# Kernel tuning notes

Hardware: AMD Instinct MI355X
Metric: run time of the kernel (lower is better)

The kernel has to match this reference:

```python
import jax, jax.numpy as jnp
import numpy as np

RADIUS = 4
SIGMA1 = 5.0
SIGMA2 = 1.0


def _gauss_1d(radius, sigma):
    x = jnp.arange(-radius, radius + 1, dtype=jnp.float32)
    return jnp.exp(-(x ** 2) / (2.0 * sigma ** 2))  # peak-1 gaussian (norm.pdf(d)/norm.pdf(0))


def _blur3d(x, g, radius):
    # Separable 3D gaussian conv; product of 1D kernels == exp(-(dx^2+dy^2+dz^2)/(2*sigma^2)),
    # mathematically identical to the dense (2r+1)^3 conv3d in the torch module.
    dn = ('NCDHW', 'OIDHW', 'NCDHW')
    for ax in range(3):
        shape = [1, 1, 1, 1, 1]
        shape[2 + ax] = g.shape[0]
        k = g.reshape(shape)
        pad = [(0, 0), (0, 0), (0, 0)]
        pad[ax] = (radius, radius)
        x = jax.lax.conv_general_dilated(x, k, (1, 1, 1), pad, dimension_numbers=dn)
    return x


def setup_inputs() -> dict:
    key = jax.random.key(0)
    k1, k2 = jax.random.split(key)
    labels = jax.random.uniform(k1, (2, 4, 128, 128, 128), dtype=jnp.float32)
    inputs = jax.random.normal(k2, (2, 1, 128, 128, 128), dtype=jnp.float32)
    return {"labels": labels, "inputs": inputs}


def reference(labels, inputs):
    num_classes = labels.shape[1]
    g = _gauss_1d(RADIUS, SIGMA1)
    loss = jnp.float32(0.0)
    for k in range(num_classes):
        class_probs = labels[:, k:k + 1]  # [B,1,D,H,W]
        class_mean = (jnp.mean(inputs * class_probs, axis=(2, 3, 4), keepdims=True)
                      / (jnp.mean(class_probs, axis=(2, 3, 4), keepdims=True) + 1e-5))  # [B,C,1,1,1]
        diff = jnp.sum((inputs - class_mean) ** 2, axis=1, keepdims=True)  # [B,1,D,H,W]
        weights = jnp.exp(-(diff ** 2) / (SIGMA2 ** 2))
        numerator = jnp.sum(class_probs * _blur3d(class_probs * weights, g, RADIUS))
        denominator = jnp.sum(class_probs * _blur3d(weights, g, RADIUS))
        # L1Loss(x, 0) on a scalar == |x|
        loss = loss + jnp.abs(numerator / (denominator + 1e-6))
    return num_classes - loss
```

## Files before the change

### kernel.cpp

```cpp
#include <hip/hip_runtime.h>
#include <math.h>

#define DIM   128
#define SLICE (DIM*DIM)
#define VOL   (DIM*DIM*DIM)
#define NK    4
#define NVOL  8
#define SSTR  33

__constant__ float c_g[9] = {
    0.72614904f, 0.83527021f, 0.92311635f, 0.98019867f, 1.0f,
    0.98019867f, 0.92311635f, 0.83527021f, 0.72614904f
};


__global__ __launch_bounds__(256) void k_sums(
    const float* __restrict__ labels, const float* __restrict__ inputs,
    float* __restrict__ red)
{
    const int b     = blockIdx.x >> 9;
    const int chunk = blockIdx.x & 511;
    const int t     = threadIdx.x;
    const size_t off4 = (size_t)chunk*1024 + t;
    const float4* __restrict__ I4 = (const float4*)inputs + (size_t)b*(VOL/4) + off4;
    const float4* __restrict__ L4 = (const float4*)labels;
    float sp[4] = {0,0,0,0}, sip[4] = {0,0,0,0};
    #pragma unroll
    for (int j = 0; j < 4; ++j) {
        const float4 iv = I4[j*256];
        #pragma unroll
        for (int k = 0; k < 4; ++k) {
            const float4 p = L4[(size_t)(b*NK + k)*(VOL/4) + off4 + j*256];
            sp[k]  += p.x + p.y + p.z + p.w;
            sip[k] += p.x*iv.x + p.y*iv.y + p.z*iv.z + p.w*iv.w;
        }
    }
    #pragma unroll
    for (int k = 0; k < 4; ++k) {
        #pragma unroll
        for (int o = 32; o; o >>= 1) {
            sp[k]  += __shfl_down(sp[k],  o);
            sip[k] += __shfl_down(sip[k], o);
        }
    }
    __shared__ float sB[8][4];
    const int wid = t >> 6;
    if ((t & 63) == 0) {
        #pragma unroll
        for (int k = 0; k < 4; ++k) { sB[k][wid] = sp[k]; sB[4+k][wid] = sip[k]; }
    }
    __syncthreads();
    if (t < 8) {
        const float v = sB[t][0] + sB[t][1] + sB[t][2] + sB[t][3];
        atomicAdd(&red[(t < 4 ? 0 : 8) + b*NK + (t & 3)], v);
    }
}

__global__ __launch_bounds__(256) void k_fused(
    const float* __restrict__ labels, const float* __restrict__ inputs,
    const float* __restrict__ red, float* __restrict__ nd)
{
    __shared__ float4 sW[2][16*SSTR + 8];
    __shared__ float sN[4], sD[4];

    const int dq    = blockIdx.x & 3;
    const int strip = (blockIdx.x >> 2) & 15;
    const int vol   = blockIdx.x >> 6;
    const int b = vol >> 2, kcls = vol & 3;
    const int d0 = dq * 32;
    const int t  = threadIdx.x;
    const float g1 = c_g[5], g2 = c_g[6], g3 = c_g[7], g4 = c_g[8];
    const float4 z4 = make_float4(0.f, 0.f, 0.f, 0.f);

    const float* __restrict__ src = labels + (size_t)vol*VOL;
    const float mean = red[8+vol] / (red[vol] + 20.97152f);

    const int r0 = t >> 5, c0 = t & 31;
    const int r1 = r0 + 8;
    const int ho = t >> 5, wq = t & 31;

    const int hA = strip*8 - 4 + r0;
    const int hB = strip*8 - 4 + r1;
    const bool vA = (unsigned)hA < 128u;
    const bool vB = (unsigned)hB < 128u;
    const float4* __restrict__ rowA = (const float4*)(src + (size_t)(vA ? hA : 0)*DIM);
    const float4* __restrict__ rowB = (const float4*)(src + (size_t)(vB ? hB : 0)*DIM);

    const size_t ob4 = (size_t)(strip*8 + ho)*(DIM/4) + wq;
    const float4* __restrict__ P4 = (const float4*)src + ob4;
    const float4* __restrict__ I4 = (const float4*)(inputs + (size_t)b*VOL) + ob4;

    float4 ring[9];
    #pragma unroll
    for (int i = 0; i < 9; ++i) ring[i] = z4;
    float numAcc = 0.f, denAcc = 0.f;

    auto ldA = [&](int s, float4& pv, float4& cv, float4& nx) {
        pv = cv = nx = z4;
        if (vA && (unsigned)s < 128u) {
            const float4* rp = rowA + (size_t)s*(SLICE/4);
            cv = rp[c0];
            if (c0 > 0)  pv = rp[c0-1];
            if (c0 < 31) nx = rp[c0+1];
        }
    };
    auto ldB = [&](int s, float4& pv, float4& cv, float4& nx) {
        pv = cv = nx = z4;
        if (vB && (unsigned)s < 128u) {
            const float4* rp = rowB + (size_t)s*(SLICE/4);
            cv = rp[c0];
            if (c0 > 0)  pv = rp[c0-1];
            if (c0 < 31) nx = rp[c0+1];
        }
    };

    float4 Apv, Acv, Anx, Bpv, Bcv, Bnx;
    ldA(d0-4, Apv, Acv, Anx);
    ldB(d0-4, Bpv, Bcv, Bnx);

    #pragma unroll 2
    for (int s = d0-4; s < d0+36; ++s) {
        const float4 apv=Apv, acv=Acv, anx=Anx, bpv=Bpv, bcv=Bcv, bnx=Bnx;
        ldA(s+1, Apv, Acv, Anx);
        ldB(s+1, Bpv, Bcv, Bnx);
        float4 pc = z4, ic = z4;
        const bool outStep = (s >= d0+4);
        if (outStep) {
            pc = P4[(size_t)(s-4)*(SLICE/4)];
            ic = I4[(size_t)(s-4)*(SLICE/4)];
        }
        const int buf = s & 1;
        {
            float4 o;
            o.x = acv.x + g1*(apv.w+acv.y) + g2*(apv.z+acv.z) + g3*(apv.y+acv.w) + g4*(apv.x+anx.x);
            o.y = acv.y + g1*(acv.x+acv.z) + g2*(apv.w+acv.w) + g3*(apv.z+anx.x) + g4*(apv.y+anx.y);
            o.z = acv.z + g1*(acv.y+acv.w) + g2*(acv.x+anx.x) + g3*(apv.w+anx.y) + g4*(apv.z+anx.z);
            o.w = acv.w + g1*(acv.z+anx.x) + g2*(acv.y+anx.y) + g3*(acv.x+anx.z) + g4*(apv.w+anx.w);
            sW[buf][r0*SSTR + c0] = o;
        }
        {
            float4 o;
            o.x = bcv.x + g1*(bpv.w+bcv.y) + g2*(bpv.z+bcv.z) + g3*(bpv.y+bcv.w) + g4*(bpv.x+bnx.x);
            o.y = bcv.y + g1*(bcv.x+bcv.z) + g2*(bpv.w+bcv.w) + g3*(bpv.z+bnx.x) + g4*(bpv.y+bnx.y);
            o.z = bcv.z + g1*(bcv.y+bcv.w) + g2*(bcv.x+bnx.x) + g3*(bpv.w+bnx.y) + g4*(bpv.z+bnx.z);
            o.w = bcv.w + g1*(bcv.z+bnx.x) + g2*(bcv.y+bnx.y) + g3*(bcv.x+bnx.z) + g4*(bpv.w+bnx.w);
            sW[buf][r1*SSTR + c0] = o;
        }
        __syncthreads();
        float4 acc = sW[buf][(ho+4)*SSTR + wq];
        #pragma unroll
        for (int dt = 1; dt <= 4; ++dt) {
            const float g = c_g[4+dt];
            const float4 u = sW[buf][(ho+4-dt)*SSTR + wq];
            const float4 v = sW[buf][(ho+4+dt)*SSTR + wq];
            acc.x += g*(u.x+v.x); acc.y += g*(u.y+v.y);
            acc.z += g*(u.z+v.z); acc.w += g*(u.w+v.w);
        }
        #pragma unroll
        for (int i = 0; i < 8; ++i) ring[i] = ring[i+1];
        ring[8] = acc;
        if (outStep) {
            float4 B = ring[4];
            #pragma unroll
            for (int dt = 1; dt <= 4; ++dt) {
                const float g = c_g[4+dt];
                B.x += g*(ring[4+dt].x + ring[4-dt].x);
                B.y += g*(ring[4+dt].y + ring[4-dt].y);
                B.z += g*(ring[4+dt].z + ring[4-dt].z);
                B.w += g*(ring[4+dt].w + ring[4-dt].w);
            }
            { float df = ic.x - mean; df *= df; const float bw = B.x * __expf(-df*df); numAcc += bw*pc.x; denAcc += bw; }
            { float df = ic.y - mean; df *= df; const float bw = B.y * __expf(-df*df); numAcc += bw*pc.y; denAcc += bw; }
            { float df = ic.z - mean; df *= df; const float bw = B.z * __expf(-df*df); numAcc += bw*pc.z; denAcc += bw; }
            { float df = ic.w - mean; df *= df; const float bw = B.w * __expf(-df*df); numAcc += bw*pc.w; denAcc += bw; }
        }
    }

    #pragma unroll
    for (int o = 32; o; o >>= 1) { numAcc += __shfl_down(numAcc, o); denAcc += __shfl_down(denAcc, o); }
    if ((t & 63) == 0) { sN[t >> 6] = numAcc; sD[t >> 6] = denAcc; }
    __syncthreads();
    if (t == 0) {
        atomicAdd(&nd[kcls],   sN[0]+sN[1]+sN[2]+sN[3]);
        atomicAdd(&nd[4+kcls], sD[0]+sD[1]+sD[2]+sD[3]);
    }
}

__global__ void k_final(const float* __restrict__ red, float* __restrict__ out)
{
    float loss = 0.f;
    #pragma unroll
    for (int k = 0; k < 4; ++k) loss += fabsf(red[16+k] / (red[20+k] + 1e-6f));
    out[0] = (float)NK - loss;
}

extern "C" void kernel_launch(void* const* d_in, const int* in_sizes, int n_in,
                              void* d_out, int out_size, void* d_ws, size_t ws_size,
                              hipStream_t stream)
{
    const float* labels = (const float*)d_in[0];
    const float* inputs = (const float*)d_in[1];
    float* out = (float*)d_out;
    float* red = (float*)d_ws;

    hipMemsetAsync(red, 0, 24*sizeof(float), stream);
    k_sums<<<2*512, 256, 0, stream>>>(labels, inputs, red);
    k_fused<<<NVOL*16*4, 256, 0, stream>>>(labels, inputs, red, red + 16);
    k_final<<<1, 1, 0, stream>>>(red, out);
}
```

Before: 184.6 us.

## Replace atomic sums with partials plus reduce kernel, lighter LDS barrier, occupancy hint

The first reduction pass now writes per-block partial sums to workspace, and a new single-block kernel combines them, replacing 8 global atomics per block. In the fused blur kernel, __syncthreads is replaced with a waitcnt-on-LDS-only plus s_barrier, so outstanding global prefetch loads need not drain at each step. A launch-bounds occupancy hint of 4 blocks per CU is also added. The cost is an extra kernel launch, and the hint may limit registers and cause spills.

```diff
diff --git a/kernel.cpp b/kernel.cpp
--- a/kernel.cpp
+++ b/kernel.cpp
@@ -13,10 +13,15 @@
     0.98019867f, 0.92311635f, 0.83527021f, 0.72614904f
 };
 
+__device__ __forceinline__ void lds_barrier() {
+    __builtin_amdgcn_s_waitcnt(0xC07F);
+    __builtin_amdgcn_s_barrier();
+}
+
 
 __global__ __launch_bounds__(256) void k_sums(
     const float* __restrict__ labels, const float* __restrict__ inputs,
-    float* __restrict__ red)
+    float* __restrict__ partials)
 {
     const int b     = blockIdx.x >> 9;
     const int chunk = blockIdx.x & 511;
@@ -50,13 +55,32 @@
         for (int k = 0; k < 4; ++k) { sB[k][wid] = sp[k]; sB[4+k][wid] = sip[k]; }
     }
     __syncthreads();
-    if (t < 8) {
-        const float v = sB[t][0] + sB[t][1] + sB[t][2] + sB[t][3];
-        atomicAdd(&red[(t < 4 ? 0 : 8) + b*NK + (t & 3)], v);
-    }
-}
-
-__global__ __launch_bounds__(256) void k_fused(
+    if (t < 8) partials[blockIdx.x*8 + t] = sB[t][0] + sB[t][1] + sB[t][2] + sB[t][3];
+}
+
+__global__ void k_reduce(const float* __restrict__ partials, float* __restrict__ red)
+{
+    __shared__ float sB[16][16];
+    const int t = threadIdx.x;
+    const int s = t & 15;
+    const int i = t >> 4;
+    const int b = s >> 3, j = s & 7;
+    float acc = 0.f;
+    for (int c = i; c < 512; c += 16)
+        acc += partials[(size_t)(b*512 + c)*8 + j];
+    sB[s][i] = acc;
+    __syncthreads();
+    if (t < 16) {
+        float v = 0.f;
+        #pragma unroll
+        for (int q = 0; q < 16; ++q) v += sB[t][q];
+        const int bb = t >> 3, jj = t & 7;
+        const int vol = bb*NK + (jj & 3);
+        red[(jj < 4 ? vol : 8 + vol)] = v;
+    }
+}
+
+__global__ __launch_bounds__(256, 4) void k_fused(
     const float* __restrict__ labels, const float* __restrict__ inputs,
     const float* __restrict__ red, float* __restrict__ nd)
 {
@@ -146,7 +170,7 @@
             o.w = bcv.w + g1*(bcv.z+bnx.x) + g2*(bcv.y+bnx.y) + g3*(bcv.x+bnx.z) + g4*(bpv.w+bnx.w);
             sW[buf][r1*SSTR + c0] = o;
         }
-        __syncthreads();
+        lds_barrier();
         float4 acc = sW[buf][(ho+4)*SSTR + wq];
         #pragma unroll
         for (int dt = 1; dt <= 4; ++dt) {
@@ -202,9 +226,11 @@
     const float* inputs = (const float*)d_in[1];
     float* out = (float*)d_out;
     float* red = (float*)d_ws;
-
-    hipMemsetAsync(red, 0, 24*sizeof(float), stream);
-    k_sums<<<2*512, 256, 0, stream>>>(labels, inputs, red);
+    float* partials = red + 32;
+
+    hipMemsetAsync(red + 16, 0, 8*sizeof(float), stream);
+    k_sums<<<2*512, 256, 0, stream>>>(labels, inputs, partials);
+    k_reduce<<<1, 256, 0, stream>>>(partials, red);
     k_fused<<<NVOL*16*4, 256, 0, stream>>>(labels, inputs, red, red + 16);
     k_final<<<1, 1, 0, stream>>>(red, out);
 }
```

New measurement: 215.9 us. +17.0%, slower.

## Process two depth slices per barrier with quad-buffered shared tile

Applied to the files above, without the earlier changes.

Restructures the depth sweep so each iteration blurs and stages two consecutive slices into four shared buffers, halving the number of block barriers, and issues loads for the next two slices ahead. It also adds launch bounds requesting four blocks per CU. The aim is to cut synchronisation overhead and expose more memory-level parallelism. In exchange it needs more registers for the extra in-flight windows and a wider ring, which the occupancy hint may force into spills.

```diff
diff --git a/kernel.cpp b/kernel.cpp
--- a/kernel.cpp
+++ b/kernel.cpp
@@ -56,11 +56,11 @@
     }
 }
 
-__global__ __launch_bounds__(256) void k_fused(
+__global__ __launch_bounds__(256, 4) void k_fused(
     const float* __restrict__ labels, const float* __restrict__ inputs,
     const float* __restrict__ red, float* __restrict__ nd)
 {
-    __shared__ float4 sW[2][16*SSTR + 8];
+    __shared__ float4 sW[4][16*SSTR];
     __shared__ float sN[4], sD[4];
 
     const int dq    = blockIdx.x & 3;
@@ -76,11 +76,10 @@
     const float mean = red[8+vol] / (red[vol] + 20.97152f);
 
     const int r0 = t >> 5, c0 = t & 31;
-    const int r1 = r0 + 8;
     const int ho = t >> 5, wq = t & 31;
 
     const int hA = strip*8 - 4 + r0;
-    const int hB = strip*8 - 4 + r1;
+    const int hB = strip*8 + 4 + r0;
     const bool vA = (unsigned)hA < 128u;
     const bool vB = (unsigned)hB < 128u;
     const float4* __restrict__ rowA = (const float4*)(src + (size_t)(vA ? hA : 0)*DIM);
@@ -90,12 +89,7 @@
     const float4* __restrict__ P4 = (const float4*)src + ob4;
     const float4* __restrict__ I4 = (const float4*)(inputs + (size_t)b*VOL) + ob4;
 
-    float4 ring[9];
-    #pragma unroll
-    for (int i = 0; i < 9; ++i) ring[i] = z4;
-    float numAcc = 0.f, denAcc = 0.f;
-
-    auto ldA = [&](int s, float4& pv, float4& cv, float4& nx) {
+    auto winA = [&](int s, float4& pv, float4& cv, float4& nx) {
         pv = cv = nx = z4;
         if (vA && (unsigned)s < 128u) {
             const float4* rp = rowA + (size_t)s*(SLICE/4);
@@ -104,7 +98,7 @@
             if (c0 < 31) nx = rp[c0+1];
         }
     };
-    auto ldB = [&](int s, float4& pv, float4& cv, float4& nx) {
+    auto winB = [&](int s, float4& pv, float4& cv, float4& nx) {
         pv = cv = nx = z4;
         if (vB && (unsigned)s < 128u) {
             const float4* rp = rowB + (size_t)s*(SLICE/4);
@@ -113,40 +107,15 @@
             if (c0 < 31) nx = rp[c0+1];
         }
     };
-
-    float4 Apv, Acv, Anx, Bpv, Bcv, Bnx;
-    ldA(d0-4, Apv, Acv, Anx);
-    ldB(d0-4, Bpv, Bcv, Bnx);
-
-    #pragma unroll 2
-    for (int s = d0-4; s < d0+36; ++s) {
-        const float4 apv=Apv, acv=Acv, anx=Anx, bpv=Bpv, bcv=Bcv, bnx=Bnx;
-        ldA(s+1, Apv, Acv, Anx);
-        ldB(s+1, Bpv, Bcv, Bnx);
-        float4 pc = z4, ic = z4;
-        const bool outStep = (s >= d0+4);
-        if (outStep) {
-            pc = P4[(size_t)(s-4)*(SLICE/4)];
-            ic = I4[(size_t)(s-4)*(SLICE/4)];
-        }
-        const int buf = s & 1;
-        {
-            float4 o;
-            o.x = acv.x + g1*(apv.w+acv.y) + g2*(apv.z+acv.z) + g3*(apv.y+acv.w) + g4*(apv.x+anx.x);
-            o.y = acv.y + g1*(acv.x+acv.z) + g2*(apv.w+acv.w) + g3*(apv.z+anx.x) + g4*(apv.y+anx.y);
-            o.z = acv.z + g1*(acv.y+acv.w) + g2*(acv.x+anx.x) + g3*(apv.w+anx.y) + g4*(apv.z+anx.z);
-            o.w = acv.w + g1*(acv.z+anx.x) + g2*(acv.y+anx.y) + g3*(acv.x+anx.z) + g4*(apv.w+anx.w);
-            sW[buf][r0*SSTR + c0] = o;
-        }
-        {
-            float4 o;
-            o.x = bcv.x + g1*(bpv.w+bcv.y) + g2*(bpv.z+bcv.z) + g3*(bpv.y+bcv.w) + g4*(bpv.x+bnx.x);
-            o.y = bcv.y + g1*(bcv.x+bcv.z) + g2*(bpv.w+bcv.w) + g3*(bpv.z+bnx.x) + g4*(bpv.y+bnx.y);
-            o.z = bcv.z + g1*(bcv.y+bcv.w) + g2*(bcv.x+bnx.x) + g3*(bpv.w+bnx.y) + g4*(bpv.z+bnx.z);
-            o.w = bcv.w + g1*(bcv.z+bnx.x) + g2*(bcv.y+bnx.y) + g3*(bcv.x+bnx.z) + g4*(bpv.w+bnx.w);
-            sW[buf][r1*SSTR + c0] = o;
-        }
-        __syncthreads();
+    auto wblur = [&](const float4& pv, const float4& cv, const float4& nx) -> float4 {
+        float4 o;
+        o.x = cv.x + g1*(pv.w+cv.y) + g2*(pv.z+cv.z) + g3*(pv.y+cv.w) + g4*(pv.x+nx.x);
+        o.y = cv.y + g1*(cv.x+cv.z) + g2*(pv.w+cv.w) + g3*(pv.z+nx.x) + g4*(pv.y+nx.y);
+        o.z = cv.z + g1*(cv.y+cv.w) + g2*(cv.x+nx.x) + g3*(pv.w+nx.y) + g4*(pv.z+nx.z);
+        o.w = cv.w + g1*(cv.z+nx.x) + g2*(cv.y+nx.y) + g3*(cv.x+nx.z) + g4*(pv.w+nx.w);
+        return o;
+    };
+    auto hblur = [&](int buf) -> float4 {
         float4 acc = sW[buf][(ho+4)*SSTR + wq];
         #pragma unroll
         for (int dt = 1; dt <= 4; ++dt) {
@@ -156,23 +125,63 @@
             acc.x += g*(u.x+v.x); acc.y += g*(u.y+v.y);
             acc.z += g*(u.z+v.z); acc.w += g*(u.w+v.w);
         }
-        #pragma unroll
-        for (int i = 0; i < 8; ++i) ring[i] = ring[i+1];
-        ring[8] = acc;
+        return acc;
+    };
+
+    float4 ring[10];
+    #pragma unroll
+    for (int i = 0; i < 10; ++i) ring[i] = z4;
+    float numAcc = 0.f, denAcc = 0.f;
+
+    float4 a0p,a0c,a0n, a1p,a1c,a1n, b0p,b0c,b0n, b1p,b1c,b1n;
+    winA(d0-4, a0p,a0c,a0n);  winA(d0-3, a1p,a1c,a1n);
+    winB(d0-4, b0p,b0c,b0n);  winB(d0-3, b1p,b1c,b1n);
+
+    for (int p = 0; p < 20; ++p) {
+        const int s0 = d0 - 4 + 2*p;
+        const int buf0 = (p & 1)*2, buf1 = buf0 + 1;
+        sW[buf0][r0*SSTR + c0]     = wblur(a0p,a0c,a0n);
+        sW[buf1][r0*SSTR + c0]     = wblur(a1p,a1c,a1n);
+        sW[buf0][(r0+8)*SSTR + c0] = wblur(b0p,b0c,b0n);
+        sW[buf1][(r0+8)*SSTR + c0] = wblur(b1p,b1c,b1n);
+        if (p < 19) {
+            winA(s0+2, a0p,a0c,a0n);  winA(s0+3, a1p,a1c,a1n);
+            winB(s0+2, b0p,b0c,b0n);  winB(s0+3, b1p,b1c,b1n);
+        }
+        float4 pc0 = z4, ic0 = z4, pc1 = z4, ic1 = z4;
+        const bool outStep = (p >= 4);
         if (outStep) {
-            float4 B = ring[4];
+            pc0 = P4[(size_t)(s0-4)*(SLICE/4)];  ic0 = I4[(size_t)(s0-4)*(SLICE/4)];
+            pc1 = P4[(size_t)(s0-3)*(SLICE/4)];  ic1 = I4[(size_t)(s0-3)*(SLICE/4)];
+        }
+        __syncthreads();
+        const float4 acc0 = hblur(buf0);
+        const float4 acc1 = hblur(buf1);
+        #pragma unroll
+        for (int i = 0; i < 8; ++i) ring[i] = ring[i+2];
+        ring[8] = acc0;  ring[9] = acc1;
+        if (outStep) {
+            float4 B0 = ring[4], B1 = ring[5];
             #pragma unroll
             for (int dt = 1; dt <= 4; ++dt) {
                 const float g = c_g[4+dt];
-                B.x += g*(ring[4+dt].x + ring[4-dt].x);
-                B.y += g*(ring[4+dt].y + ring[4-dt].y);
-                B.z += g*(ring[4+dt].z + ring[4-dt].z);
-                B.w += g*(ring[4+dt].w + ring[4-dt].w);
+                B0.x += g*(ring[4+dt].x + ring[4-dt].x);
+                B0.y += g*(ring[4+dt].y + ring[4-dt].y);
+                B0.z += g*(ring[4+dt].z + ring[4-dt].z);
+                B0.w += g*(ring[4+dt].w + ring[4-dt].w);
+                B1.x += g*(ring[5+dt].x + ring[5-dt].x);
+                B1.y += g*(ring[5+dt].y + ring[5-dt].y);
+                B1.z += g*(ring[5+dt].z + ring[5-dt].z);
+                B1.w += g*(ring[5+dt].w + ring[5-dt].w);
             }
-            { float df = ic.x - mean; df *= df; const float bw = B.x * __expf(-df*df); numAcc += bw*pc.x; denAcc += bw; }
-            { float df = ic.y - mean; df *= df; const float bw = B.y * __expf(-df*df); numAcc += bw*pc.y; denAcc += bw; }
-            { float df = ic.z - mean; df *= df; const float bw = B.z * __expf(-df*df); numAcc += bw*pc.z; denAcc += bw; }
-            { float df = ic.w - mean; df *= df; const float bw = B.w * __expf(-df*df); numAcc += bw*pc.w; denAcc += bw; }
+            { float df = ic0.x - mean; df *= df; const float bw = B0.x * __expf(-df*df); numAcc += bw*pc0.x; denAcc += bw; }
+            { float df = ic0.y - mean; df *= df; const float bw = B0.y * __expf(-df*df); numAcc += bw*pc0.y; denAcc += bw; }
+            { float df = ic0.z - mean; df *= df; const float bw = B0.z * __expf(-df*df); numAcc += bw*pc0.z; denAcc += bw; }
+            { float df = ic0.w - mean; df *= df; const float bw = B0.w * __expf(-df*df); numAcc += bw*pc0.w; denAcc += bw; }
+            { float df = ic1.x - mean; df *= df; const float bw = B1.x * __expf(-df*df); numAcc += bw*pc1.x; denAcc += bw; }
+            { float df = ic1.y - mean; df *= df; const float bw = B1.y * __expf(-df*df); numAcc += bw*pc1.y; denAcc += bw; }
+            { float df = ic1.z - mean; df *= df; const float bw = B1.z * __expf(-df*df); numAcc += bw*pc1.z; denAcc += bw; }
+            { float df = ic1.w - mean; df *= df; const float bw = B1.w * __expf(-df*df); numAcc += bw*pc1.w; denAcc += bw; }
         }
     }
 
```

Result: slower. 346.2 us (+87.6%).
